# Kernel tuning notes

Hardware: AMD Instinct MI355X
Metric: run time of the kernel (lower is better)

Reference implementation:

```python
import jax, jax.numpy as jnp
import numpy as np

B, C, HW = 128, 3, 224
P = 16
D = 256
NH = 8
HD = D // NH
E = 4            # num_experts
K = 2            # top-k
FF = 4 * D
NC = 38
EPS = 1e-5


def _layernorm(x, g, b):
    mu = jnp.mean(x, axis=-1, keepdims=True)
    var = jnp.mean(jnp.square(x - mu), axis=-1, keepdims=True)
    return (x - mu) * jax.lax.rsqrt(var + EPS) * g + b


def setup_inputs() -> dict:
    key = jax.random.key(0)
    ks = jax.random.split(key, 16)
    s = 0.02
    return {
        "x": jax.random.normal(ks[0], (B, C, HW, HW), dtype=jnp.float32),
        "conv_w": jax.random.normal(ks[1], (D, C, P, P), dtype=jnp.float32) * s,
        "conv_b": jnp.zeros((D,), jnp.float32),
        "cls_token": jnp.zeros((1, 1, D), jnp.float32),
        "ln1_g": jnp.ones((D,), jnp.float32),
        "ln1_b": jnp.zeros((D,), jnp.float32),
        "qkv_w": jax.random.normal(ks[2], (3 * D, D), dtype=jnp.float32) * s,
        "qkv_b": jnp.zeros((3 * D,), jnp.float32),
        "out_w": jax.random.normal(ks[3], (D, D), dtype=jnp.float32) * s,
        "out_b": jnp.zeros((D,), jnp.float32),
        "ln2_g": jnp.ones((D,), jnp.float32),
        "ln2_b": jnp.zeros((D,), jnp.float32),
        "router_w": jax.random.normal(ks[4], (E, D), dtype=jnp.float32) * s,
        "router_b": jnp.zeros((E,), jnp.float32),
        "e_w1": jax.random.normal(ks[5], (E, D, FF), dtype=jnp.float32) * s,
        "e_b1": jnp.zeros((E, FF), jnp.float32),
        "e_w2": jax.random.normal(ks[6], (E, FF, D), dtype=jnp.float32) * s,
        "e_b2": jnp.zeros((E, D), jnp.float32),
        "head_w": jax.random.normal(ks[7], (NC, D), dtype=jnp.float32) * s,
        "head_b": jnp.zeros((NC,), jnp.float32),
    }


def reference(x, conv_w, conv_b, cls_token, ln1_g, ln1_b, qkv_w, qkv_b,
              out_w, out_b, ln2_g, ln2_b, router_w, router_b,
              e_w1, e_b1, e_w2, e_b2, head_w, head_b):
    # patch embed: Conv2d(3, D, 16, 16) -> [B, D, 14, 14] -> [B, 196, D]
    h = jax.lax.conv_general_dilated(
        x, conv_w, window_strides=(P, P), padding="VALID",
        dimension_numbers=("NCHW", "OIHW", "NCHW")) + conv_b[None, :, None, None]
    b = h.shape[0]
    tok = h.reshape(b, D, -1).transpose(0, 2, 1)            # [B, 196, D]
    tok = jnp.concatenate([jnp.broadcast_to(cls_token, (b, 1, D)), tok], axis=1)  # [B, 197, D]
    S = tok.shape[1]

    # Multi-head self-attention (pre-norm)
    x2 = _layernorm(tok, ln1_g, ln1_b)
    qkv = x2 @ qkv_w.T + qkv_b                              # [B, S, 3D]
    q, k, v = jnp.split(qkv, 3, axis=-1)
    q = q.reshape(b, S, NH, HD)
    k = k.reshape(b, S, NH, HD)
    v = v.reshape(b, S, NH, HD)
    scores = jnp.einsum("bqhd,bkhd->bhqk", q, k) / np.float32(np.sqrt(HD))
    attn = jax.nn.softmax(scores, axis=-1)
    ao = jnp.einsum("bhqk,bkhd->bqhd", attn, v).reshape(b, S, D)
    ao = ao @ out_w.T + out_b
    tok = tok + ao

    # MoE FFN (pre-norm). NOTE: original code computes top-k routing weights
    # but never multiplies outputs by them — outputs of selected experts are
    # simply summed. We reproduce that faithfully.
    x2 = _layernorm(tok, ln2_g, ln2_b)
    x_flat = x2.reshape(-1, D)                              # [T, D]
    logits = x_flat @ router_w.T + router_b                 # [T, E]
    probs = jax.nn.softmax(logits, axis=-1)
    _topw, topi = jax.lax.top_k(probs, K)                   # topw unused (as in source)
    mask = (topi[..., None] == jnp.arange(E)).any(axis=1)   # [T, E] bool
    out_flat = jnp.zeros_like(x_flat)
    for i in range(E):                                       # fixed small expert count
        hid = jax.nn.gelu(x_flat @ e_w1[i] + e_b1[i], approximate=False)
        out_flat = out_flat + mask[:, i:i + 1].astype(x_flat.dtype) * (hid @ e_w2[i] + e_b2[i])
    tok = tok + out_flat.reshape(b, S, D)

    return tok[:, 0] @ head_w.T + head_b                    # [B, NC]
```

## Files before the change

kernel.cpp:

```cpp
#include <hip/hip_runtime.h>
#include <hip/hip_bf16.h>
#include <math.h>

#define TTOK   25216
#define SEQL   197
#define NBATCH 128
#define DMODEL 256
#define NHEADS 8
#define FFD    1024
#define NEXP   4
#define NCLS   38
#define CONVK  768
#define NPATCH 196
#define CM     25088

typedef unsigned short u16;
typedef unsigned int u32;
using s16x4 = __attribute__((ext_vector_type(4))) short;
using s16x8 = __attribute__((ext_vector_type(8))) short;
using f32x4 = __attribute__((ext_vector_type(4))) float;

__device__ __forceinline__ float b2f(u16 v) {
  union { unsigned u; float f; } x; x.u = (unsigned)v << 16; return x.f;
}
__device__ __forceinline__ u16 f2b(float f) {
  __hip_bfloat16 h = __float2bfloat16(f);
  return *reinterpret_cast<u16*>(&h);
}
__device__ __forceinline__ void gload16(const void* g, void* l) {
  __builtin_amdgcn_global_load_lds(
      (const __attribute__((address_space(1))) void*)g,
      (__attribute__((address_space(3))) void*)l, 16, 0, 0);
}
__device__ __forceinline__ float warp_sum(float v) {
  #pragma unroll
  for (int o = 32; o; o >>= 1) v += __shfl_xor(v, o);
  return v;
}
__device__ __forceinline__ float warp_max(float v) {
  #pragma unroll
  for (int o = 32; o; o >>= 1) v = fmaxf(v, __shfl_xor(v, o));
  return v;
}
__device__ __forceinline__ int fsw(int row) { return (row ^ (row >> 2)) & 3; }
__device__ __forceinline__ s16x8 ldA72(const u16* base, int rowa, int l4) {
  const char* p = (const char*)base + rowa * 72 + l4 * 16;
  s16x4 a = *(const s16x4*)p;
  s16x4 b = *(const s16x4*)(p + 8);
  return __builtin_shufflevector(a, b, 0, 1, 2, 3, 4, 5, 6, 7);
}

__global__ __launch_bounds__(256) void k_cast2b(const float* __restrict__ cw,
                                                u16* __restrict__ cwh,
                                                u16* __restrict__ cwl,
                                                const float* __restrict__ qw,
                                                u16* __restrict__ qwh,
                                                u16* __restrict__ qwl,
                                                const float* __restrict__ cls,
                                                const float* __restrict__ ln1g,
                                                const float* __restrict__ ln1b,
                                                const float* __restrict__ qb,
                                                float* __restrict__ qf) {
  int bid = blockIdx.x;
  if (bid == 384) {
    const int n = threadIdx.x, w = n >> 6, lane = n & 63;
    __shared__ float xs[DMODEL];
    __shared__ float red[8];
    float v = cls[n];
    float s1 = warp_sum(v), s2 = warp_sum(v * v);
    if (lane == 0) { red[w] = s1; red[4 + w] = s2; }
    __syncthreads();
    s1 = red[0] + red[1] + red[2] + red[3];
    s2 = red[4] + red[5] + red[6] + red[7];
    float mu = s1 * (1.f / DMODEL);
    float var = s2 * (1.f / DMODEL) - mu * mu;
    float rs = rsqrtf(var + 1e-5f);
    xs[n] = (v - mu) * rs * ln1g[n] + ln1b[n];
    __syncthreads();
    float val = qb[n];
    #pragma unroll 4
    for (int i = 0; i < 64; ++i) {
      float4 wv = *(const float4*)(qw + (size_t)n * DMODEL + i * 4);
      val = fmaf(wv.x, xs[i * 4 + 0], val);
      val = fmaf(wv.y, xs[i * 4 + 1], val);
      val = fmaf(wv.z, xs[i * 4 + 2], val);
      val = fmaf(wv.w, xs[i * 4 + 3], val);
    }
    qf[n] = val;
    return;
  }
  const float* in = cw; u16* hi = cwh; u16* lo = cwl;
  if (bid >= 192) { bid -= 192; in = qw; hi = qwh; lo = qwl; }
  int i = (bid * 256 + threadIdx.x) * 4;
  float4 v = *(const float4*)&in[i];
  float vv[4] = {v.x, v.y, v.z, v.w};
  u16 h[4], l[4];
  #pragma unroll
  for (int j = 0; j < 4; ++j) {
    h[j] = f2b(vv[j]);
    l[j] = f2b(vv[j] - b2f(h[j]));
  }
  *(uint2*)&hi[i] = *(const uint2*)h;
  *(uint2*)&lo[i] = *(const uint2*)l;
}

__global__ __launch_bounds__(256) void k_conv(const float* __restrict__ x,
                                              const u16* __restrict__ cwh,
                                              const u16* __restrict__ cwl,
                                              const float* __restrict__ cb,
                                              float* __restrict__ tok) {
  const int n0 = blockIdx.x * 128;
  const int m0 = blockIdx.y * 128;
  __shared__ __align__(16) u16 lds[25600];
  u16* Ah_s = lds;
  u16* Al_s = lds + 4608;
  u16* Wbuf = lds + 9216;
  const int tid = threadIdx.x;
  const int lane = tid & 63;
  const int wv = tid >> 6;
  const int wr = wv >> 1, wc = wv & 1;
  const int l15 = lane & 15, l4 = lane >> 4;
  f32x4 acc[4][4] = {};

  const int kpos = (tid & 7) * 4;
  long abase[4]; int aldso[4];
  #pragma unroll
  for (int it = 0; it < 4; ++it) {
    int row = it * 32 + (tid >> 3);
    int m = m0 + row;
    int b = m / NPATCH, p = m - b * NPATCH;
    int py = p / 14, px = p - py * 14;
    abase[it] = (long)(b * 3) * 50176 + (py * 16) * 224 + px * 16;
    aldso[it] = row * 72 + kpos * 2;
  }
  long woff[2]; int wofs[2];
  #pragma unroll
  for (int r = 0; r < 2; ++r) {
    int off = r * 4096 + tid * 16;
    int row = off >> 6;
    int c16 = (off >> 4) & 3;
    int kk = (c16 ^ fsw(row)) << 3;
    woff[r] = (long)(n0 + row) * CONVK + kk;
    wofs[r] = off;
  }
  #pragma unroll
  for (int r = 0; r < 2; ++r) {
    gload16(cwh + woff[r], (char*)Wbuf + wofs[r]);
    gload16(cwl + woff[r], (char*)Wbuf + 8192 + wofs[r]);
  }
  float4 xr[4];
  {
    int c = kpos >> 8, r8 = kpos & 255;
    long soff = (long)c * 50176 + (r8 >> 4) * 224 + (r8 & 15);
    #pragma unroll
    for (int it = 0; it < 4; ++it) xr[it] = *(const float4*)&x[abase[it] + soff];
  }
  int cur = 0;
  for (int kc = 0; kc < CONVK; kc += 32) {
    #pragma unroll
    for (int it = 0; it < 4; ++it) {
      float vv[4] = {xr[it].x, xr[it].y, xr[it].z, xr[it].w};
      u16 h[4], l[4];
      #pragma unroll
      for (int j = 0; j < 4; ++j) {
        h[j] = f2b(vv[j]);
        l[j] = f2b(vv[j] - b2f(h[j]));
      }
      *(uint2*)((char*)Ah_s + aldso[it]) = *(const uint2*)h;
      *(uint2*)((char*)Al_s + aldso[it]) = *(const uint2*)l;
    }
    __syncthreads();
    if (kc + 32 < CONVK) {
      char* wdst = (char*)Wbuf + ((cur ^ 1) << 14);
      #pragma unroll
      for (int r = 0; r < 2; ++r) {
        gload16(cwh + woff[r] + kc + 32, wdst + wofs[r]);
        gload16(cwl + woff[r] + kc + 32, wdst + 8192 + wofs[r]);
      }
      int k = kc + 32 + kpos;
      int c = k >> 8, r8 = k & 255;
      long soff = (long)c * 50176 + (r8 >> 4) * 224 + (r8 & 15);
      #pragma unroll
      for (int it = 0; it < 4; ++it) xr[it] = *(const float4*)&x[abase[it] + soff];
    }
    const char* Wcur = (const char*)Wbuf + (cur << 14);
    s16x8 ah[4], al[4], bh[4], bl[4];
    #pragma unroll
    for (int i = 0; i < 4; ++i) {
      int rowa = wr * 64 + i * 16 + l15;
      ah[i] = ldA72(Ah_s, rowa, l4);
      al[i] = ldA72(Al_s, rowa, l4);
      int rowb = wc * 64 + i * 16 + l15;
      int kbb = (l4 ^ fsw(rowb)) << 4;
      bh[i] = *(const s16x8*)(Wcur + rowb * 64 + kbb);
      bl[i] = *(const s16x8*)(Wcur + 8192 + rowb * 64 + kbb);
    }
    #pragma unroll
    for (int i = 0; i < 4; ++i)
      #pragma unroll
      for (int j = 0; j < 4; ++j)
        acc[i][j] = __builtin_amdgcn_mfma_f32_16x16x32_bf16(ah[i], bh[j],
                                                            acc[i][j], 0, 0, 0);
    #pragma unroll
    for (int i = 0; i < 4; ++i)
      #pragma unroll
      for (int j = 0; j < 4; ++j)
        acc[i][j] = __builtin_amdgcn_mfma_f32_16x16x32_bf16(ah[i], bl[j],
                                                            acc[i][j], 0, 0, 0);
    #pragma unroll
    for (int i = 0; i < 4; ++i)
      #pragma unroll
      for (int j = 0; j < 4; ++j)
        acc[i][j] = __builtin_amdgcn_mfma_f32_16x16x32_bf16(al[i], bh[j],
                                                            acc[i][j], 0, 0, 0);
    __syncthreads();
    cur ^= 1;
  }
  const int mb = m0 + wr * 64 + (l4 << 2);
  const int nb = n0 + wc * 64 + l15;
  #pragma unroll
  for (int i = 0; i < 4; ++i) {
    #pragma unroll
    for (int jf = 0; jf < 4; ++jf) {
      #pragma unroll
      for (int j = 0; j < 4; ++j) {
        int m = mb + i * 16 + j;
        int n = nb + jf * 16;
        int bq = m / NPATCH;
        long cr = (long)bq * SEQL + (m - bq * NPATCH) + 1;
        tok[cr * DMODEL + n] = acc[i][jf][j] + cb[n];
      }
    }
  }
}

__global__ __launch_bounds__(256) void k_lnstat(const float* __restrict__ cls,
                                                float* __restrict__ tok,
                                                float2* __restrict__ st) {
  const int row = blockIdx.x * 4 + (threadIdx.x >> 6);
  const int lane = threadIdx.x & 63;
  const int b = row / SEQL, s = row - b * SEQL;
  float vv[4];
  if (s == 0) {
    *(float4*)vv = *(const float4*)&cls[lane * 4];
    *(float4*)&tok[(size_t)row * DMODEL + lane * 4] = *(const float4*)vv;
  } else {
    *(float4*)vv = *(const float4*)&tok[(size_t)row * DMODEL + lane * 4];
  }
  float s1 = vv[0] + vv[1] + vv[2] + vv[3];
  float s2 = vv[0]*vv[0] + vv[1]*vv[1] + vv[2]*vv[2] + vv[3]*vv[3];
  s1 = warp_sum(s1);
  s2 = warp_sum(s2);
  if (lane == 0) {
    float mu = s1 * (1.f / DMODEL);
    float var = s2 * (1.f / DMODEL) - mu * mu;
    st[row] = make_float2(mu, rsqrtf(var + 1e-5f));
  }
}

__global__ __launch_bounds__(256) void k_qkv(const float* __restrict__ tok,
                                             const float2* __restrict__ stats,
                                             const float* __restrict__ g,
                                             const float* __restrict__ bb,
                                             const u16* __restrict__ Wh,
                                             const u16* __restrict__ Wl,
                                             const float* __restrict__ bias,
                                             float* __restrict__ Cf) {
  const int n0 = blockIdx.x * 128;
  const int m0 = blockIdx.y * 128;
  __shared__ __align__(16) u16 lds[25600];
  u16* Ah_s = lds;
  u16* Al_s = lds + 4608;
  u16* Wbuf = lds + 9216;
  const int tid = threadIdx.x;
  const int lane = tid & 63;
  const int wv = tid >> 6;
  const int wr = wv >> 1, wc = wv & 1;
  const int l15 = lane & 15, l4 = lane >> 4;
  f32x4 acc[4][4] = {};

  const int kpos = (tid & 7) * 4;
  long atok[4]; float2 st[4]; int aldso[4];
  #pragma unroll
  for (int it = 0; it < 4; ++it) {
    int row = it * 32 + (tid >> 3);
    int m = m0 + row;
    atok[it] = (long)m * DMODEL;
    st[it] = stats[m];
    aldso[it] = row * 72 + kpos * 2;
  }
  long woff[2]; int wofs[2];
  #pragma unroll
  for (int r = 0; r < 2; ++r) {
    int off = r * 4096 + tid * 16;
    int row = off >> 6;
    int c16 = (off >> 4) & 3;
    int kk = (c16 ^ fsw(row)) << 3;
    woff[r] = (long)(n0 + row) * DMODEL + kk;
    wofs[r] = off;
  }
  #pragma unroll
  for (int r = 0; r < 2; ++r) {
    gload16(Wh + woff[r], (char*)Wbuf + wofs[r]);
    gload16(Wl + woff[r], (char*)Wbuf + 8192 + wofs[r]);
  }
  float4 xr[4], gr, br;
  #pragma unroll
  for (int it = 0; it < 4; ++it) xr[it] = *(const float4*)&tok[atok[it] + kpos];
  gr = *(const float4*)&g[kpos];
  br = *(const float4*)&bb[kpos];
  int cur = 0;
  for (int kc = 0; kc < DMODEL; kc += 32) {
    float gg[4] = {gr.x, gr.y, gr.z, gr.w};
    float bbv[4] = {br.x, br.y, br.z, br.w};
    #pragma unroll
    for (int it = 0; it < 4; ++it) {
      float vv[4] = {xr[it].x, xr[it].y, xr[it].z, xr[it].w};
      u16 h[4], l[4];
      #pragma unroll
      for (int j = 0; j < 4; ++j) {
        float xd = (vv[j] - st[it].x) * st[it].y * gg[j] + bbv[j];
        h[j] = f2b(xd);
        l[j] = f2b(xd - b2f(h[j]));
      }
      *(uint2*)((char*)Ah_s + aldso[it]) = *(const uint2*)h;
      *(uint2*)((char*)Al_s + aldso[it]) = *(const uint2*)l;
    }
    __syncthreads();
    if (kc + 32 < DMODEL) {
      char* wdst = (char*)Wbuf + ((cur ^ 1) << 14);
      #pragma unroll
      for (int r = 0; r < 2; ++r) {
        gload16(Wh + woff[r] + kc + 32, wdst + wofs[r]);
        gload16(Wl + woff[r] + kc + 32, wdst + 8192 + wofs[r]);
      }
      #pragma unroll
      for (int it = 0; it < 4; ++it)
        xr[it] = *(const float4*)&tok[atok[it] + kc + 32 + kpos];
      gr = *(const float4*)&g[kc + 32 + kpos];
      br = *(const float4*)&bb[kc + 32 + kpos];
    }
    const char* Wcur = (const char*)Wbuf + (cur << 14);
    s16x8 ah[4], al[4], bh[4], bl[4];
    #pragma unroll
    for (int i = 0; i < 4; ++i) {
      int rowa = wr * 64 + i * 16 + l15;
      ah[i] = ldA72(Ah_s, rowa, l4);
      al[i] = ldA72(Al_s, rowa, l4);
      int rowb = wc * 64 + i * 16 + l15;
      int kbb = (l4 ^ fsw(rowb)) << 4;
      bh[i] = *(const s16x8*)(Wcur + rowb * 64 + kbb);
      bl[i] = *(const s16x8*)(Wcur + 8192 + rowb * 64 + kbb);
    }
    #pragma unroll
    for (int i = 0; i < 4; ++i)
      #pragma unroll
      for (int j = 0; j < 4; ++j)
        acc[i][j] = __builtin_amdgcn_mfma_f32_16x16x32_bf16(ah[i], bh[j],
                                                            acc[i][j], 0, 0, 0);
    #pragma unroll
    for (int i = 0; i < 4; ++i)
      #pragma unroll
      for (int j = 0; j < 4; ++j)
        acc[i][j] = __builtin_amdgcn_mfma_f32_16x16x32_bf16(ah[i], bl[j],
                                                            acc[i][j], 0, 0, 0);
    #pragma unroll
    for (int i = 0; i < 4; ++i)
      #pragma unroll
      for (int j = 0; j < 4; ++j)
        acc[i][j] = __builtin_amdgcn_mfma_f32_16x16x32_bf16(al[i], bh[j],
                                                            acc[i][j], 0, 0, 0);
    __syncthreads();
    cur ^= 1;
  }
  const int mb = m0 + wr * 64 + (l4 << 2);
  const int nb = n0 + wc * 64 + l15;
  #pragma unroll
  for (int i = 0; i < 4; ++i) {
    #pragma unroll
    for (int jf = 0; jf < 4; ++jf) {
      #pragma unroll
      for (int j = 0; j < 4; ++j) {
        int m = mb + i * 16 + j;
        int n = nb + jf * 16;
        Cf[(long)m * 512 + n] = acc[i][jf][j] + bias[n];
      }
    }
  }
}

__global__ __launch_bounds__(512) void k_attn_tail(
    const float* __restrict__ qf, const float* __restrict__ kvf,
    const float* __restrict__ ow, const float* __restrict__ ob,
    const float* __restrict__ cls,
    const float* __restrict__ g, const float* __restrict__ bb,
    const float* __restrict__ rw, const float* __restrict__ rb,
    const float* __restrict__ w1, const float* __restrict__ b1,
    float* __restrict__ tokc, float* __restrict__ maskf,
    float* __restrict__ hid) {
  const int b = blockIdx.x;
  const int tid = threadIdx.x, w = tid >> 6, lane = tid & 63;
  __shared__ float Ss[8][200];
  __shared__ float aos[DMODEL];
  __shared__ float xd_s[DMODEL];
  __shared__ float red[8];
  __shared__ float lg[4];
  __shared__ float mk[4];
  __shared__ int epair[2];

  const int h = w;
  float q[32];
  #pragma unroll
  for (int i = 0; i < 8; ++i) {
    float4 q4 = *(const float4*)(qf + h * 32 + i * 4);
    q[i * 4 + 0] = q4.x; q[i * 4 + 1] = q4.y;
    q[i * 4 + 2] = q4.z; q[i * 4 + 3] = q4.w;
  }
  float sc[4];
  float mx = -1e30f;
  #pragma unroll
  for (int r = 0; r < 4; ++r) {
    int k = lane + 64 * r;
    float s = -1e30f;
    if (k < SEQL) {
      const float* kr = kvf + ((size_t)(b * SEQL + k)) * 512 + h * 32;
      s = 0.f;
      #pragma unroll
      for (int i = 0; i < 8; ++i) {
        float4 kv4 = *(const float4*)(kr + i * 4);
        s = fmaf(kv4.x, q[i * 4 + 0], s);
        s = fmaf(kv4.y, q[i * 4 + 1], s);
        s = fmaf(kv4.z, q[i * 4 + 2], s);
        s = fmaf(kv4.w, q[i * 4 + 3], s);
      }
      s *= 0.17677669529663687f;
    }
    sc[r] = s;
    mx = fmaxf(mx, s);
  }
  mx = warp_max(mx);
  float sm = 0.f;
  #pragma unroll
  for (int r = 0; r < 4; ++r) {
    int k = lane + 64 * r;
    float e = (k < SEQL) ? __expf(sc[r] - mx) : 0.f;
    sc[r] = e;
    sm += e;
  }
  sm = warp_sum(sm);
  float inv = 1.f / sm;
  #pragma unroll
  for (int r = 0; r < 4; ++r) {
    int k = lane + 64 * r;
    if (k < SEQL) Ss[w][k] = sc[r] * inv;
  }
  int d = lane & 31, half = lane >> 5;
  float pv = 0.f;
  for (int i = 0; i < 99; ++i) {
    int k = half * 99 + i;
    if (k < SEQL)
      pv = fmaf(Ss[w][k], kvf[((size_t)(b * SEQL + k)) * 512 + 256 + h * 32 + d], pv);
  }
  pv += __shfl_xor(pv, 32);
  if (lane < 32) aos[h * 32 + d] = pv;
  __syncthreads();

  float t_ = 0.f;
  if (tid < 256) {
    float val = ob[tid];
    #pragma unroll 4
    for (int i = 0; i < 64; ++i) {
      float4 wv2 = *(const float4*)(ow + (size_t)tid * DMODEL + i * 4);
      val = fmaf(wv2.x, aos[i * 4 + 0], val);
      val = fmaf(wv2.y, aos[i * 4 + 1], val);
      val = fmaf(wv2.z, aos[i * 4 + 2], val);
      val = fmaf(wv2.w, aos[i * 4 + 3], val);
    }
    t_ = cls[tid] + val;
    tokc[b * DMODEL + tid] = t_;
  }
  float s1 = warp_sum(t_), s2 = warp_sum(t_ * t_);
  if (tid < 256 && lane == 0) { red[w] = s1; red[4 + w] = s2; }
  __syncthreads();
  s1 = red[0] + red[1] + red[2] + red[3];
  s2 = red[4] + red[5] + red[6] + red[7];
  float mu = s1 * (1.f / DMODEL);
  float var = s2 * (1.f / DMODEL) - mu * mu;
  float rs = rsqrtf(var + 1e-5f);
  if (tid < 256) xd_s[tid] = (t_ - mu) * rs * g[tid] + bb[tid];
  __syncthreads();

  if (tid < 256) {
    float s = 0.f;
    #pragma unroll
    for (int i = 0; i < 4; ++i)
      s = fmaf(xd_s[lane + i * 64], rw[w * DMODEL + lane + i * 64], s);
    s = warp_sum(s) + rb[w];
    if (lane == 0) lg[w] = s;
  }
  __syncthreads();
  if (tid < NEXP) {
    int e = tid;
    int rank = 0;
    #pragma unroll
    for (int j = 0; j < NEXP; ++j)
      if (j != e && (lg[j] > lg[e] || (lg[j] == lg[e] && j < e))) ++rank;
    float m = (rank < 2) ? 1.f : 0.f;
    mk[e] = m;
    maskf[b * NEXP + e] = m;
  }
  __syncthreads();
  if (tid == 0) {
    int e0 = 0;
    while (e0 < 3 && mk[e0] == 0.f) ++e0;
    int e1 = e0 + 1;
    while (e1 < 3 && mk[e1] == 0.f) ++e1;
    epair[0] = e0; epair[1] = e1;
  }
  __syncthreads();

  const int e0 = epair[0], e1 = epair[1];
  const float* w1a = w1 + (size_t)e0 * DMODEL * FFD + tid;
  const float* w1b = w1 + (size_t)e1 * DMODEL * FFD + tid;
  float a0 = 0.f, a1 = 0.f, a2 = 0.f, a3 = 0.f;
  #pragma unroll 4
  for (int k = 0; k < DMODEL; ++k) {
    float xv = xd_s[k];
    const float* ra = w1a + (size_t)k * FFD;
    const float* rb2 = w1b + (size_t)k * FFD;
    a0 = fmaf(xv, ra[0], a0);
    a1 = fmaf(xv, ra[512], a1);
    a2 = fmaf(xv, rb2[0], a2);
    a3 = fmaf(xv, rb2[512], a3);
  }
  float* h0 = hid + ((size_t)e0 * NBATCH + b) * FFD;
  float* h1 = hid + ((size_t)e1 * NBATCH + b) * FFD;
  float v0 = a0 + b1[e0 * FFD + tid];
  float v1 = a1 + b1[e0 * FFD + tid + 512];
  float v2 = a2 + b1[e1 * FFD + tid];
  float v3 = a3 + b1[e1 * FFD + tid + 512];
  h0[tid]       = 0.5f * v0 * (1.0f + erff(v0 * 0.70710678118654752f));
  h0[tid + 512] = 0.5f * v1 * (1.0f + erff(v1 * 0.70710678118654752f));
  h1[tid]       = 0.5f * v2 * (1.0f + erff(v2 * 0.70710678118654752f));
  h1[tid + 512] = 0.5f * v3 * (1.0f + erff(v3 * 0.70710678118654752f));
}

__global__ __launch_bounds__(256) void k_moe2(const float* __restrict__ hid,
                                              const float* __restrict__ w2,
                                              const float* __restrict__ b2,
                                              const float* __restrict__ maskf,
                                              float* __restrict__ tokc) {
  const int t = blockIdx.x, dc = blockIdx.y;
  const int tid = threadIdx.x;
  const int dl = tid & 127, kh = tid >> 7;
  const int dout = dc * 128 + dl;
  int e0 = 0;
  while (e0 < 3 && maskf[t * NEXP + e0] == 0.f) ++e0;
  int e1 = e0 + 1;
  while (e1 < 3 && maskf[t * NEXP + e1] == 0.f) ++e1;
  __shared__ float hs0[FFD], hs1[FFD];
  const float* h0 = hid + ((size_t)e0 * NBATCH + t) * FFD;
  const float* h1 = hid + ((size_t)e1 * NBATCH + t) * FFD;
  for (int i = tid * 4; i < FFD; i += 1024) {
    *(float4*)&hs0[i] = *(const float4*)&h0[i];
    *(float4*)&hs1[i] = *(const float4*)&h1[i];
  }
  __syncthreads();
  const float* w20 = w2 + (size_t)e0 * FFD * DMODEL + dout;
  const float* w21 = w2 + (size_t)e1 * FFD * DMODEL + dout;
  float a0 = 0.f, a1 = 0.f;
  const int k0 = kh * 512;
  #pragma unroll 8
  for (int k = k0; k < k0 + 512; ++k) {
    a0 = fmaf(hs0[k], w20[(size_t)k * DMODEL], a0);
    a1 = fmaf(hs1[k], w21[(size_t)k * DMODEL], a1);
  }
  __shared__ float red[256];
  red[tid] = a0 + a1;
  __syncthreads();
  if (kh == 0) {
    float full = red[dl] + red[128 + dl] +
                 b2[e0 * DMODEL + dout] + b2[e1 * DMODEL + dout];
    tokc[t * DMODEL + dout] += full;
  }
}

__global__ __launch_bounds__(256) void k_head(const float* __restrict__ tokc,
                                              const float* __restrict__ hw,
                                              const float* __restrict__ hb,
                                              float* __restrict__ out) {
  int b = blockIdx.x;
  int w = threadIdx.x >> 6, lane = threadIdx.x & 63;
  const float* row = tokc + (size_t)b * DMODEL;
  for (int c = w; c < NCLS; c += 4) {
    float s = 0.f;
    for (int d = lane; d < DMODEL; d += 64) s = fmaf(row[d], hw[c * DMODEL + d], s);
    s = warp_sum(s);
    if (lane == 0) out[b * NCLS + c] = s + hb[c];
  }
}

extern "C" void kernel_launch(void* const* d_in, const int* in_sizes, int n_in,
                              void* d_out, int out_size, void* d_ws, size_t ws_size,
                              hipStream_t stream) {
  const float* x      = (const float*)d_in[0];
  const float* conv_w = (const float*)d_in[1];
  const float* conv_b = (const float*)d_in[2];
  const float* cls    = (const float*)d_in[3];
  const float* ln1g   = (const float*)d_in[4];
  const float* ln1b   = (const float*)d_in[5];
  const float* qkv_w  = (const float*)d_in[6];
  const float* qkv_b  = (const float*)d_in[7];
  const float* out_w  = (const float*)d_in[8];
  const float* out_b  = (const float*)d_in[9];
  const float* ln2g   = (const float*)d_in[10];
  const float* ln2b   = (const float*)d_in[11];
  const float* rw     = (const float*)d_in[12];
  const float* rb     = (const float*)d_in[13];
  const float* e_w1   = (const float*)d_in[14];
  const float* e_b1   = (const float*)d_in[15];
  const float* e_w2   = (const float*)d_in[16];
  const float* e_b2   = (const float*)d_in[17];
  const float* head_w = (const float*)d_in[18];
  const float* head_b = (const float*)d_in[19];
  float* out = (float*)d_out;

  char* ws = (char*)d_ws;
  size_t off = 0;
  auto alloc = [&](size_t bytes) {
    void* p = ws + off;
    off += (bytes + 255) & ~(size_t)255;
    return p;
  };
  float*  tok   = (float*)alloc((size_t)TTOK * DMODEL * 4);
  float*  qkvf  = (float*)alloc((size_t)TTOK * 512 * 4);
  float2* stats = (float2*)alloc((size_t)TTOK * 8);
  u16*    cwh   = (u16*)alloc((size_t)DMODEL * CONVK * 2);
  u16*    cwl   = (u16*)alloc((size_t)DMODEL * CONVK * 2);
  u16*    qwh   = (u16*)alloc((size_t)768 * DMODEL * 2);
  u16*    qwl   = (u16*)alloc((size_t)768 * DMODEL * 2);
  float*  qf    = (float*)alloc((size_t)DMODEL * 4);
  float*  tokc  = (float*)alloc((size_t)NBATCH * DMODEL * 4);
  float*  maskf = (float*)alloc((size_t)NBATCH * NEXP * 4);
  float*  hid   = (float*)alloc((size_t)NEXP * NBATCH * FFD * 4);

  k_cast2b<<<385, 256, 0, stream>>>(conv_w, cwh, cwl, qkv_w, qwh, qwl,
                                    cls, ln1g, ln1b, qkv_b, qf);

  k_conv<<<dim3(2, CM / 128), 256, 0, stream>>>(x, cwh, cwl, conv_b, tok);

  k_lnstat<<<TTOK / 4, 256, 0, stream>>>(cls, tok, stats);

  k_qkv<<<dim3(4, TTOK / 128), 256, 0, stream>>>(
      tok, stats, ln1g, ln1b, qwh + 256 * DMODEL, qwl + 256 * DMODEL,
      qkv_b + 256, qkvf);

  k_attn_tail<<<NBATCH, 512, 0, stream>>>(qf, qkvf, out_w, out_b, cls,
                                          ln2g, ln2b, rw, rb,
                                          e_w1, e_b1, tokc, maskf, hid);

  k_moe2<<<dim3(NBATCH, 2), 256, 0, stream>>>(hid, e_w2, e_b2, maskf, tokc);
  k_head<<<NBATCH, 256, 0, stream>>>(tokc, head_w, head_b, out);
}
```

Before: 201.2 us.

## Split CLS attention into separate per-(batch,head) kernel for more parallelism

Moves the CLS-query attention out of the fused tail kernel into a new kernel launched over batch×heads blocks. Each block spreads the 197 keys across 256 threads and splits the PV reduction eight ways, where before one wave per head looped serially over about 99 keys per half-wave. The goal is more blocks and shorter per-thread chains in the attention step, which was latency-bound with only 128 blocks. In exchange it adds a kernel launch and a small global round-trip for the attention output.

After: 189.9 us (median of 2 runs). -5.6%, faster.

```diff
diff --git a/kernel.cpp b/kernel.cpp
--- a/kernel.cpp
+++ b/kernel.cpp
@@ -389,8 +389,63 @@
   }
 }
 
-__global__ __launch_bounds__(512) void k_attn_tail(
-    const float* __restrict__ qf, const float* __restrict__ kvf,
+__global__ __launch_bounds__(256) void k_attn2(const float* __restrict__ qf,
+                                               const float* __restrict__ kvf,
+                                               float* __restrict__ aocf) {
+  const int b = blockIdx.x, h = blockIdx.y;
+  const int tid = threadIdx.x, w = tid >> 6, lane = tid & 63;
+  __shared__ float qs[32];
+  __shared__ float Ps[256];
+  __shared__ float red[8];
+  __shared__ float pvred[8][32];
+  if (tid < 32) qs[tid] = qf[h * 32 + tid];
+  __syncthreads();
+  float s = -1e30f;
+  if (tid < SEQL) {
+    const float* kr = kvf + ((size_t)(b * SEQL + tid)) * 512 + h * 32;
+    float a = 0.f;
+    #pragma unroll
+    for (int i = 0; i < 8; ++i) {
+      float4 k4 = *(const float4*)(kr + i * 4);
+      a = fmaf(k4.x, qs[i * 4 + 0], a);
+      a = fmaf(k4.y, qs[i * 4 + 1], a);
+      a = fmaf(k4.z, qs[i * 4 + 2], a);
+      a = fmaf(k4.w, qs[i * 4 + 3], a);
+    }
+    s = a * 0.17677669529663687f;
+  }
+  float mx = warp_max(s);
+  if (lane == 0) red[w] = mx;
+  __syncthreads();
+  mx = fmaxf(fmaxf(red[0], red[1]), fmaxf(red[2], red[3]));
+  float e = (tid < SEQL) ? __expf(s - mx) : 0.f;
+  float ssum = warp_sum(e);
+  if (lane == 0) red[4 + w] = ssum;
+  __syncthreads();
+  float inv = 1.f / (red[4] + red[5] + red[6] + red[7]);
+  Ps[tid] = e * inv;
+  __syncthreads();
+  const int d = tid & 31, kq = tid >> 5;
+  float acc = 0.f;
+  const int kbeg = kq * 25;
+  #pragma unroll 5
+  for (int i = 0; i < 25; ++i) {
+    int k = kbeg + i;
+    if (k < SEQL)
+      acc = fmaf(Ps[k], kvf[((size_t)(b * SEQL + k)) * 512 + 256 + h * 32 + d], acc);
+  }
+  pvred[kq][d] = acc;
+  __syncthreads();
+  if (tid < 32) {
+    float r = 0.f;
+    #pragma unroll
+    for (int j = 0; j < 8; ++j) r += pvred[j][tid];
+    aocf[b * DMODEL + h * 32 + tid] = r;
+  }
+}
+
+__global__ __launch_bounds__(512) void k_tail2(
+    const float* __restrict__ aocf,
     const float* __restrict__ ow, const float* __restrict__ ob,
     const float* __restrict__ cls,
     const float* __restrict__ g, const float* __restrict__ bb,
@@ -400,7 +455,6 @@
     float* __restrict__ hid) {
   const int b = blockIdx.x;
   const int tid = threadIdx.x, w = tid >> 6, lane = tid & 63;
-  __shared__ float Ss[8][200];
   __shared__ float aos[DMODEL];
   __shared__ float xd_s[DMODEL];
   __shared__ float red[8];
@@ -408,61 +462,7 @@
   __shared__ float mk[4];
   __shared__ int epair[2];
 
-  const int h = w;
-  float q[32];
-  #pragma unroll
-  for (int i = 0; i < 8; ++i) {
-    float4 q4 = *(const float4*)(qf + h * 32 + i * 4);
-    q[i * 4 + 0] = q4.x; q[i * 4 + 1] = q4.y;
-    q[i * 4 + 2] = q4.z; q[i * 4 + 3] = q4.w;
-  }
-  float sc[4];
-  float mx = -1e30f;
-  #pragma unroll
-  for (int r = 0; r < 4; ++r) {
-    int k = lane + 64 * r;
-    float s = -1e30f;
-    if (k < SEQL) {
-      const float* kr = kvf + ((size_t)(b * SEQL + k)) * 512 + h * 32;
-      s = 0.f;
-      #pragma unroll
-      for (int i = 0; i < 8; ++i) {
-        float4 kv4 = *(const float4*)(kr + i * 4);
-        s = fmaf(kv4.x, q[i * 4 + 0], s);
-        s = fmaf(kv4.y, q[i * 4 + 1], s);
-        s = fmaf(kv4.z, q[i * 4 + 2], s);
-        s = fmaf(kv4.w, q[i * 4 + 3], s);
-      }
-      s *= 0.17677669529663687f;
-    }
-    sc[r] = s;
-    mx = fmaxf(mx, s);
-  }
-  mx = warp_max(mx);
-  float sm = 0.f;
-  #pragma unroll
-  for (int r = 0; r < 4; ++r) {
-    int k = lane + 64 * r;
-    float e = (k < SEQL) ? __expf(sc[r] - mx) : 0.f;
-    sc[r] = e;
-    sm += e;
-  }
-  sm = warp_sum(sm);
-  float inv = 1.f / sm;
-  #pragma unroll
-  for (int r = 0; r < 4; ++r) {
-    int k = lane + 64 * r;
-    if (k < SEQL) Ss[w][k] = sc[r] * inv;
-  }
-  int d = lane & 31, half = lane >> 5;
-  float pv = 0.f;
-  for (int i = 0; i < 99; ++i) {
-    int k = half * 99 + i;
-    if (k < SEQL)
-      pv = fmaf(Ss[w][k], kvf[((size_t)(b * SEQL + k)) * 512 + 256 + h * 32 + d], pv);
-  }
-  pv += __shfl_xor(pv, 32);
-  if (lane < 32) aos[h * 32 + d] = pv;
+  if (tid < 256) aos[tid] = aocf[b * DMODEL + tid];
   __syncthreads();
 
   float t_ = 0.f;
@@ -640,6 +640,7 @@
   u16*    qwh   = (u16*)alloc((size_t)768 * DMODEL * 2);
   u16*    qwl   = (u16*)alloc((size_t)768 * DMODEL * 2);
   float*  qf    = (float*)alloc((size_t)DMODEL * 4);
+  float*  aocf  = (float*)alloc((size_t)NBATCH * DMODEL * 4);
   float*  tokc  = (float*)alloc((size_t)NBATCH * DMODEL * 4);
   float*  maskf = (float*)alloc((size_t)NBATCH * NEXP * 4);
   float*  hid   = (float*)alloc((size_t)NEXP * NBATCH * FFD * 4);
@@ -655,9 +656,11 @@
       tok, stats, ln1g, ln1b, qwh + 256 * DMODEL, qwl + 256 * DMODEL,
       qkv_b + 256, qkvf);
 
-  k_attn_tail<<<NBATCH, 512, 0, stream>>>(qf, qkvf, out_w, out_b, cls,
-                                          ln2g, ln2b, rw, rb,
-                                          e_w1, e_b1, tokc, maskf, hid);
+  k_attn2<<<dim3(NBATCH, NHEADS), 256, 0, stream>>>(qf, qkvf, aocf);
+
+  k_tail2<<<NBATCH, 512, 0, stream>>>(aocf, out_w, out_b, cls,
+                                      ln2g, ln2b, rw, rb,
+                                      e_w1, e_b1, tokc, maskf, hid);
 
   k_moe2<<<dim3(NBATCH, 2), 256, 0, stream>>>(hid, e_w2, e_b2, maskf, tokc);
   k_head<<<NBATCH, 256, 0, stream>>>(tokc, head_w, head_b, out);
```
